# Kernel tuning notes

Hardware: AMD Instinct MI355X
Metric: run time of the kernel (lower is better)

The kernel has to match this reference:

```python
import jax, jax.numpy as jnp
import numpy as np

D_IN, N_HEADS, N_KV, HEAD_DIM = 2048, 8, 4, 256
GROUP = N_HEADS // N_KV
SCALING = 256.0 ** -0.5  # query_pre_attn_scalar = 256
EPS = 1e-6


def _rms_norm(x, gamma):
    # Gemma-style RMSNorm with (1 + gamma) scale, over last dim (head_dim)
    var = jnp.mean(x * x, axis=-1, keepdims=True)
    return x * jax.lax.rsqrt(var + EPS) * (1.0 + gamma)


def _apply_rope(x, cos, sin):
    # x: [b, h, s, d]; cos/sin: [s, d] (rotate-half convention)
    d = x.shape[-1]
    x1, x2 = x[..., : d // 2], x[..., d // 2:]
    rotated = jnp.concatenate([-x2, x1], axis=-1)
    return x * cos[None, None] + rotated * sin[None, None]


def setup_inputs() -> dict:
    key = jax.random.key(0)
    ks = jax.random.split(key, 6)
    b, s = 2, 2048
    x = jax.random.normal(ks[0], (b, s, D_IN), dtype=jnp.float32)
    # causal mask: True above diagonal = masked
    mask = jnp.triu(jnp.ones((s, s), dtype=bool), k=1)
    # RoPE tables (base 10000)
    inv_freq = 1.0 / (10000.0 ** (jnp.arange(0, HEAD_DIM, 2, dtype=jnp.float32) / HEAD_DIM))
    angles = jnp.arange(s, dtype=jnp.float32)[:, None] * inv_freq[None, :]  # [s, d/2]
    angles = jnp.concatenate([angles, angles], axis=-1)  # [s, d]
    cos, sin = jnp.cos(angles), jnp.sin(angles)
    std = 0.02
    wq = jax.random.normal(ks[1], (N_HEADS * HEAD_DIM, D_IN), dtype=jnp.float32) * std
    wk = jax.random.normal(ks[2], (N_KV * HEAD_DIM, D_IN), dtype=jnp.float32) * std
    wv = jax.random.normal(ks[3], (N_KV * HEAD_DIM, D_IN), dtype=jnp.float32) * std
    wo = jax.random.normal(ks[4], (D_IN, N_HEADS * HEAD_DIM), dtype=jnp.float32) * std
    q_gamma = jnp.zeros((HEAD_DIM,), dtype=jnp.float32)
    k_gamma = jnp.zeros((HEAD_DIM,), dtype=jnp.float32)
    return {"x": x, "mask": mask, "cos": cos, "sin": sin,
            "wq": wq, "wk": wk, "wv": wv, "wo": wo,
            "q_gamma": q_gamma, "k_gamma": k_gamma}


def reference(x, mask, cos, sin, wq, wk, wv, wo, q_gamma, k_gamma):
    b, s, _ = x.shape
    # projections (torch Linear: y = x @ W.T)
    q = (x @ wq.T).reshape(b, s, N_HEADS, HEAD_DIM).transpose(0, 2, 1, 3)  # [b,H,s,d]
    k = (x @ wk.T).reshape(b, s, N_KV, HEAD_DIM).transpose(0, 2, 1, 3)     # [b,G,s,d]
    v = (x @ wv.T).reshape(b, s, N_KV, HEAD_DIM).transpose(0, 2, 1, 3)     # [b,G,s,d]
    q = _rms_norm(q, q_gamma)
    k = _rms_norm(k, k_gamma)
    q = _apply_rope(q, cos, sin) * SCALING
    k = _apply_rope(k, cos, sin)
    # GQA via broadcast (avoids repeat_interleave): head h = g*GROUP + j (group-major)
    qg = q.reshape(b, N_KV, GROUP, s, HEAD_DIM)
    scores = jnp.einsum('bgjqd,bgkd->bgjqk', qg, k)  # [b,G,group,s,s]
    scores = jnp.where(mask[None, None, None], -jnp.inf, scores)
    weights = jax.nn.softmax(scores, axis=-1)
    ctx = jnp.einsum('bgjqk,bgkd->bgjqd', weights, v)  # [b,G,group,s,d]
    ctx = ctx.reshape(b, N_HEADS, s, HEAD_DIM).transpose(0, 2, 1, 3).reshape(b, s, N_HEADS * HEAD_DIM)
    return ctx @ wo.T
```

## Files before the change

kernel.cpp:

```cpp
#include <hip/hip_runtime.h>
#include <math.h>


typedef __bf16 bf16x8 __attribute__((ext_vector_type(8)));
typedef __bf16 bf16x4 __attribute__((ext_vector_type(4)));
typedef float  f32x4  __attribute__((ext_vector_type(4)));

#define MFMA16(a, b, c) __builtin_amdgcn_mfma_f32_16x16x32_bf16(a, b, c, 0, 0, 0)

__device__ __forceinline__ void async16(const __bf16* g, const __bf16* l) {
  __builtin_amdgcn_global_load_lds(
      (__attribute__((address_space(1))) const void*)g,
      (__attribute__((address_space(3))) void*)l, 16, 0, 0);
}

__global__ __launch_bounds__(256) void cast_f32_bf16(
    const float* __restrict__ src, __bf16* __restrict__ dst) {
  const size_t i = ((size_t)blockIdx.x * 256 + threadIdx.x) * 4;
  f32x4 v = *(const f32x4*)(src + i);
  bf16x4 o;
#pragma unroll
  for (int j = 0; j < 4; j++) o[j] = (__bf16)v[j];
  *(bf16x4*)(dst + i) = o;
}

template <typename OT>
__device__ __forceinline__ void gemm_body(const __bf16* A, const __bf16* B,
                                          OT* C, size_t m0, size_t n0,
                                          size_t ccol0, int ldc) {
  constexpr int K = 2048;
  __shared__ __align__(16) __bf16 As[128 * 32];
  __shared__ __align__(16) __bf16 Bs[128 * 32];
  const int tid = threadIdx.x;
  const int wave = tid >> 6, lane = tid & 63;
  const int lr = lane & 15, lq = lane >> 4;
  const int wm = (wave >> 1) * 64, wn = (wave & 1) * 64;

  f32x4 acc[4][4];
#pragma unroll
  for (int i = 0; i < 4; i++)
#pragma unroll
    for (int j = 0; j < 4; j++)
#pragma unroll
      for (int r = 0; r < 4; r++) acc[i][j][r] = 0.f;

  int srow[2], skof[2];
#pragma unroll
  for (int c = 0; c < 2; c++) {
    const int t = wave * 2 + c;
    const int g = t * 8 + (lane >> 3);
    const int cc = (lane & 7) ^ (g & 7);
    srow[c] = g * 2 + (cc >> 2);
    skof[c] = (cc & 3) * 8;
  }

  for (int k0 = 0; k0 < K; k0 += 32) {
#pragma unroll
    for (int c = 0; c < 2; c++) {
      const int t = wave * 2 + c;
      async16(A + (m0 + srow[c]) * K + k0 + skof[c], As + t * 512);
      async16(B + (n0 + srow[c]) * K + k0 + skof[c], Bs + t * 512);
    }
    __syncthreads();
    bf16x8 af[4], bf[4];
#pragma unroll
    for (int i = 0; i < 4; i++) {
      const int row = wm + i * 16 + lr;
      const int g = row >> 1;
      const int p = ((row & 1) * 4 + lq) ^ (g & 7);
      af[i] = *(const bf16x8*)&As[g * 64 + p * 8];
    }
#pragma unroll
    for (int j = 0; j < 4; j++) {
      const int row = wn + j * 16 + lr;
      const int g = row >> 1;
      const int p = ((row & 1) * 4 + lq) ^ (g & 7);
      bf[j] = *(const bf16x8*)&Bs[g * 64 + p * 8];
    }
#pragma unroll
    for (int i = 0; i < 4; i++)
#pragma unroll
      for (int j = 0; j < 4; j++)
        acc[i][j] = MFMA16(af[i], bf[j], acc[i][j]);
    __syncthreads();
  }

#pragma unroll
  for (int i = 0; i < 4; i++)
#pragma unroll
    for (int j = 0; j < 4; j++)
#pragma unroll
      for (int r = 0; r < 4; r++) {
        const size_t row = m0 + wm + i * 16 + lq * 4 + r;
        const size_t col = ccol0 + wn + j * 16 + lr;
        C[row * (size_t)ldc + col] = (OT)acc[i][j][r];
      }
}

template <typename OT>
__global__ __launch_bounds__(256) void gemm_bt(
    const __bf16* __restrict__ A, const __bf16* __restrict__ B,
    OT* __restrict__ C, const int ldc) {
  gemm_body<OT>(A, B, C, (size_t)blockIdx.y * 128, (size_t)blockIdx.x * 128,
                (size_t)blockIdx.x * 128, ldc);
}

__global__ __launch_bounds__(256) void gemm_qkv(
    const __bf16* __restrict__ A, const __bf16* __restrict__ Bq,
    const __bf16* __restrict__ Bk, const __bf16* __restrict__ Bv,
    __bf16* __restrict__ C) {
  const int bx = blockIdx.x;
  const __bf16* B;
  int nl;
  if (bx < 16) { B = Bq; nl = bx; }
  else if (bx < 24) { B = Bk; nl = bx - 16; }
  else { B = Bv; nl = bx - 24; }
  gemm_body<__bf16>(A, B, C, (size_t)blockIdx.y * 128, (size_t)nl * 128,
                    (size_t)bx * 128, 4096);
}

__global__ __launch_bounds__(256) void rmsrope(
    const __bf16* __restrict__ qkv, const float* __restrict__ cosb,
    const float* __restrict__ sinb, const float* __restrict__ qg,
    const float* __restrict__ kg, __bf16* __restrict__ qrot,
    __bf16* __restrict__ krot) {
  const int wave = threadIdx.x >> 6, lane = threadIdx.x & 63;
  const int rid = blockIdx.x * 4 + wave;
  const int m = rid / 12, seg = rid % 12;
  const int b = m >> 11, pos = m & 2047;
  const bool isq = seg < 8;
  const int col = isq ? seg * 256 : 2048 + (seg - 8) * 256;
  const int d = lane * 4;

  bf16x4 xv = *(const bf16x4*)(qkv + (size_t)m * 4096 + col + d);
  float x[4];
#pragma unroll
  for (int i = 0; i < 4; i++) x[i] = (float)xv[i];
  float ss = x[0] * x[0] + x[1] * x[1] + x[2] * x[2] + x[3] * x[3];
#pragma unroll
  for (int off = 1; off < 64; off <<= 1) ss += __shfl_xor(ss, off);
  const float inv = rsqrtf(ss * (1.f / 256.f) + 1e-6f);

  f32x4 gv = *(const f32x4*)((isq ? qg : kg) + d);
  float xn[4];
#pragma unroll
  for (int i = 0; i < 4; i++) xn[i] = x[i] * inv * (1.f + gv[i]);
  float rot[4];
#pragma unroll
  for (int i = 0; i < 4; i++) {
    const float pn = __shfl_xor(xn[i], 32);
    rot[i] = (lane < 32) ? -pn : pn;
  }
  f32x4 cv = *(const f32x4*)(cosb + (size_t)pos * 256 + d);
  f32x4 sv = *(const f32x4*)(sinb + (size_t)pos * 256 + d);
  const float sc = isq ? 0.0625f : 1.f;
  bf16x4 ov;
#pragma unroll
  for (int i = 0; i < 4; i++)
    ov[i] = (__bf16)((xn[i] * cv[i] + rot[i] * sv[i]) * sc);
  __bf16* dst = isq
      ? qrot + ((size_t)(b * 8 + seg) * 2048 + pos) * 256 + d
      : krot + ((size_t)(b * 4 + (seg - 8)) * 2048 + pos) * 256 + d;
  *(bf16x4*)dst = ov;
}

__global__ __launch_bounds__(256) void vtrans(const __bf16* __restrict__ qkv,
                                              __bf16* __restrict__ vT) {
  __shared__ __bf16 tile[64 * 65];
  const int bkv = blockIdx.z;
  const int d0 = blockIdx.y * 64, p0 = blockIdx.x * 64;
  const int t = threadIdx.x;
  const int b = bkv >> 2, kv = bkv & 3;
#pragma unroll
  for (int i = 0; i < 16; i++) {
    const int f = i * 256 + t;
    const int pl = f >> 6, dl = f & 63;
    tile[pl * 65 + dl] =
        qkv[(size_t)(b * 2048 + p0 + pl) * 4096 + 3072 + kv * 256 + d0 + dl];
  }
  __syncthreads();
#pragma unroll
  for (int i = 0; i < 16; i++) {
    const int f = i * 256 + t;
    const int dl = f >> 6, pl = f & 63;
    vT[((size_t)bkv * 256 + d0 + dl) * 2048 + p0 + pl] = tile[pl * 65 + dl];
  }
}

__global__ __launch_bounds__(256) void flash(
    const __bf16* __restrict__ qrot, const __bf16* __restrict__ krot,
    const __bf16* __restrict__ vT, __bf16* __restrict__ ctx) {
  __shared__ __align__(16) __bf16 Ks[2][32 * 256];
  __shared__ __align__(16) __bf16 Vs[2][256 * 32];
  __shared__ __align__(16) __bf16 Ps[4 * 1024];
  const int tid = threadIdx.x, wave = tid >> 6, lane = tid & 63;
  const int lr = lane & 15, lq = lane >> 4;
  const int bkv = blockIdx.x;
  const int b = bkv >> 2, kv = bkv & 3;
  const int qt = 31 - (int)blockIdx.y;
  const int h = kv * 2 + (wave >> 1);
  const int q0 = qt * 64 + (wave & 1) * 32;

  bf16x8 qf[2][8];
  {
    const __bf16* qbb = qrot + (size_t)(b * 8 + h) * 2048 * 256;
#pragma unroll
    for (int qi = 0; qi < 2; qi++)
#pragma unroll
      for (int i = 0; i < 8; i++)
        qf[qi][i] = *(const bf16x8*)(qbb + (size_t)(q0 + qi * 16 + lr) * 256 +
                                     i * 32 + lq * 8);
  }
  f32x4 acc[2][16];
#pragma unroll
  for (int qi = 0; qi < 2; qi++)
#pragma unroll
    for (int j = 0; j < 16; j++)
#pragma unroll
      for (int r = 0; r < 4; r++) acc[qi][j][r] = 0.f;
  float lsum[2][4];
#pragma unroll
  for (int qi = 0; qi < 2; qi++)
#pragma unroll
    for (int r = 0; r < 4; r++) lsum[qi][r] = 0.f;

  const __bf16* kbase = krot + (size_t)bkv * 2048 * 256;
  const __bf16* vbase = vT + (size_t)bkv * 256 * 2048;

  int koff[4], voff[4];
#pragma unroll
  for (int c = 0; c < 4; c++) {
    const int t = wave * 4 + c;
    {
      const int row = t * 2 + (lane >> 5);
      const int ch = (lane & 31) ^ row;
      koff[c] = row * 256 + ch * 8;
    }
    {
      const int d = t * 16 + (lane >> 2);
      const int ch = (lane & 3) ^ ((d >> 1) & 3);
      voff[c] = d * 2048 + ch * 8;
    }
  }

  const int nkt = 2 * qt + 2;
#pragma unroll
  for (int c = 0; c < 4; c++) {
    const int t = wave * 4 + c;
    async16(kbase + koff[c], &Ks[0][t * 512]);
    async16(vbase + voff[c], &Vs[0][t * 512]);
  }

  for (int kt = 0; kt < nkt; kt++) {
    const int bi = kt & 1;
    const int k0 = kt * 32;
    __syncthreads();
    if (kt + 1 < nkt) {
      const int kn = (kt + 1) * 32;
#pragma unroll
      for (int c = 0; c < 4; c++) {
        const int t = wave * 4 + c;
        async16(kbase + (size_t)kn * 256 + koff[c], &Ks[bi ^ 1][t * 512]);
        async16(vbase + kn + voff[c], &Vs[bi ^ 1][t * 512]);
      }
    }
    if (k0 <= q0 + 31) {
      f32x4 s[2][2];
#pragma unroll
      for (int qi = 0; qi < 2; qi++)
#pragma unroll
        for (int f = 0; f < 2; f++)
#pragma unroll
          for (int r = 0; r < 4; r++) s[qi][f][r] = 0.f;
#pragma unroll
      for (int i = 0; i < 8; i++) {
        bf16x8 kf0 = *(const bf16x8*)&Ks[bi][lr * 256 + (((i * 4 + lq) ^ lr) * 8)];
        bf16x8 kf1 = *(const bf16x8*)&Ks[bi][(16 + lr) * 256 +
                                            (((i * 4 + lq) ^ (16 + lr)) * 8)];
#pragma unroll
        for (int qi = 0; qi < 2; qi++) {
          s[qi][0] = MFMA16(qf[qi][i], kf0, s[qi][0]);
          s[qi][1] = MFMA16(qf[qi][i], kf1, s[qi][1]);
        }
      }
      const bool needmask = (k0 + 31 > q0);
#pragma unroll
      for (int qi = 0; qi < 2; qi++) {
        const int qa = q0 + qi * 16 + lq * 4;
#pragma unroll
        for (int f = 0; f < 2; f++) {
          const int ka = k0 + f * 16 + lr;
          const int rw = qi * 16 + lq * 4;
          const int c = f * 2 + (lr >> 3);
#pragma unroll
          for (int r = 0; r < 4; r++) {
            float p = __expf(s[qi][f][r] - 16.f);
            if (needmask && ka > qa + r) p = 0.f;
            lsum[qi][r] += p;
            const int rr = rw + r;
            Ps[wave * 1024 + rr * 32 + ((c ^ ((rr >> 1) & 3)) * 8) + (lr & 7)] =
                (__bf16)p;
          }
        }
      }
      asm volatile("s_waitcnt lgkmcnt(0)" ::: "memory");
      bf16x8 pf[2];
#pragma unroll
      for (int qi = 0; qi < 2; qi++)
        pf[qi] = *(const bf16x8*)&Ps[wave * 1024 + (qi * 16 + lr) * 32 +
                                     ((lq ^ ((lr >> 1) & 3)) * 8)];
#pragma unroll
      for (int j = 0; j < 16; j++) {
        const int d = j * 16 + lr;
        bf16x8 vf =
            *(const bf16x8*)&Vs[bi][d * 32 + ((lq ^ ((d >> 1) & 3)) * 8)];
#pragma unroll
        for (int qi = 0; qi < 2; qi++)
          acc[qi][j] = MFMA16(pf[qi], vf, acc[qi][j]);
      }
    }
  }

  float inv[2][4];
#pragma unroll
  for (int qi = 0; qi < 2; qi++)
#pragma unroll
    for (int r = 0; r < 4; r++) {
      float l = lsum[qi][r];
#pragma unroll
      for (int off = 1; off < 16; off <<= 1) l += __shfl_xor(l, off);
      inv[qi][r] = 1.f / l;
    }
#pragma unroll
  for (int qi = 0; qi < 2; qi++)
#pragma unroll
    for (int j = 0; j < 16; j++)
#pragma unroll
      for (int r = 0; r < 4; r++) {
        const int row = q0 + qi * 16 + lq * 4 + r;
        ctx[((size_t)(b * 2048 + row) * 8 + h) * 256 + j * 16 + lr] =
            (__bf16)(acc[qi][j][r] * inv[qi][r]);
      }
}

extern "C" void kernel_launch(void* const* d_in, const int* in_sizes, int n_in,
                              void* d_out, int out_size, void* d_ws,
                              size_t ws_size, hipStream_t stream) {
  const float* x = (const float*)d_in[0];
  const float* cosb = (const float*)d_in[2];
  const float* sinb = (const float*)d_in[3];
  const float* wq = (const float*)d_in[4];
  const float* wk = (const float*)d_in[5];
  const float* wv = (const float*)d_in[6];
  const float* wo = (const float*)d_in[7];
  const float* qg = (const float*)d_in[8];
  const float* kg = (const float*)d_in[9];
  float* out = (float*)d_out;

  char* ws = (char*)d_ws;
  __bf16* xbf = (__bf16*)ws;
  __bf16* wqbf = (__bf16*)(ws + ((size_t)16 << 20));
  __bf16* wkbf = (__bf16*)(ws + ((size_t)24 << 20));
  __bf16* wvbf = (__bf16*)(ws + ((size_t)28 << 20));
  __bf16* qkv = (__bf16*)(ws + ((size_t)32 << 20));
  __bf16* qrot = (__bf16*)ws;
  __bf16* krot = (__bf16*)(ws + ((size_t)16 << 20));
  __bf16* vTp = (__bf16*)(ws + ((size_t)24 << 20));
  __bf16* wobf = (__bf16*)(ws + ((size_t)32 << 20));
  __bf16* ctx = (__bf16*)(ws + ((size_t)40 << 20));

  cast_f32_bf16<<<8192, 256, 0, stream>>>(x, xbf);
  cast_f32_bf16<<<4096, 256, 0, stream>>>(wq, wqbf);
  cast_f32_bf16<<<2048, 256, 0, stream>>>(wk, wkbf);
  cast_f32_bf16<<<2048, 256, 0, stream>>>(wv, wvbf);

  gemm_qkv<<<dim3(32, 32), 256, 0, stream>>>(xbf, wqbf, wkbf, wvbf, qkv);

  rmsrope<<<12288, 256, 0, stream>>>(qkv, cosb, sinb, qg, kg, qrot, krot);
  vtrans<<<dim3(32, 4, 8), 256, 0, stream>>>(qkv, vTp);

  cast_f32_bf16<<<4096, 256, 0, stream>>>(wo, wobf);
  flash<<<dim3(8, 32), 256, 0, stream>>>(qrot, krot, vTp, ctx);

  gemm_bt<float><<<dim3(16, 32), 256, 0, stream>>>(ctx, wobf, out, 2048);
}
```

Before: 479.2 us.

## Split flash blocks per query head and drop K/V double buffering

```diff
diff --git a/kernel.cpp b/kernel.cpp
--- a/kernel.cpp
+++ b/kernel.cpp
@@ -187,19 +187,17 @@
   }
 }
 
-__global__ __launch_bounds__(256) void flash(
+__global__ __launch_bounds__(128) void flash(
     const __bf16* __restrict__ qrot, const __bf16* __restrict__ krot,
     const __bf16* __restrict__ vT, __bf16* __restrict__ ctx) {
-  __shared__ __align__(16) __bf16 Ks[2][32 * 256];
-  __shared__ __align__(16) __bf16 Vs[2][256 * 32];
-  __shared__ __align__(16) __bf16 Ps[4 * 1024];
+  __shared__ __align__(16) __bf16 Ks[32 * 256];
+  __shared__ __align__(16) __bf16 Vs[256 * 32];
+  __shared__ __align__(16) __bf16 Ps[2 * 1024];
   const int tid = threadIdx.x, wave = tid >> 6, lane = tid & 63;
   const int lr = lane & 15, lq = lane >> 4;
-  const int bkv = blockIdx.x;
-  const int b = bkv >> 2, kv = bkv & 3;
-  const int qt = 31 - (int)blockIdx.y;
-  const int h = kv * 2 + (wave >> 1);
-  const int q0 = qt * 64 + (wave & 1) * 32;
+  const int qt = 31 - (int)blockIdx.x;
+  const int h = blockIdx.y, b = blockIdx.z, kv = h >> 1;
+  const int q0 = qt * 64 + wave * 32;
 
   bf16x8 qf[2][8];
   {
@@ -224,13 +222,13 @@
 #pragma unroll
     for (int r = 0; r < 4; r++) lsum[qi][r] = 0.f;
 
-  const __bf16* kbase = krot + (size_t)bkv * 2048 * 256;
-  const __bf16* vbase = vT + (size_t)bkv * 256 * 2048;
-
-  int koff[4], voff[4];
-#pragma unroll
-  for (int c = 0; c < 4; c++) {
-    const int t = wave * 4 + c;
+  const __bf16* kbase = krot + (size_t)(b * 4 + kv) * 2048 * 256;
+  const __bf16* vbase = vT + (size_t)(b * 4 + kv) * 256 * 2048;
+
+  int koff[8], voff[8];
+#pragma unroll
+  for (int c = 0; c < 8; c++) {
+    const int t = wave * 8 + c;
     {
       const int row = t * 2 + (lane >> 5);
       const int ch = (lane & 31) ^ row;
@@ -244,26 +242,15 @@
   }
 
   const int nkt = 2 * qt + 2;
-#pragma unroll
-  for (int c = 0; c < 4; c++) {
-    const int t = wave * 4 + c;
-    async16(kbase + koff[c], &Ks[0][t * 512]);
-    async16(vbase + voff[c], &Vs[0][t * 512]);
-  }
-
   for (int kt = 0; kt < nkt; kt++) {
-    const int bi = kt & 1;
     const int k0 = kt * 32;
+#pragma unroll
+    for (int c = 0; c < 8; c++) {
+      const int t = wave * 8 + c;
+      async16(kbase + (size_t)k0 * 256 + koff[c], Ks + t * 512);
+      async16(vbase + k0 + voff[c], Vs + t * 512);
+    }
     __syncthreads();
-    if (kt + 1 < nkt) {
-      const int kn = (kt + 1) * 32;
-#pragma unroll
-      for (int c = 0; c < 4; c++) {
-        const int t = wave * 4 + c;
-        async16(kbase + (size_t)kn * 256 + koff[c], &Ks[bi ^ 1][t * 512]);
-        async16(vbase + kn + voff[c], &Vs[bi ^ 1][t * 512]);
-      }
-    }
     if (k0 <= q0 + 31) {
       f32x4 s[2][2];
 #pragma unroll
@@ -274,9 +261,9 @@
           for (int r = 0; r < 4; r++) s[qi][f][r] = 0.f;
 #pragma unroll
       for (int i = 0; i < 8; i++) {
-        bf16x8 kf0 = *(const bf16x8*)&Ks[bi][lr * 256 + (((i * 4 + lq) ^ lr) * 8)];
-        bf16x8 kf1 = *(const bf16x8*)&Ks[bi][(16 + lr) * 256 +
-                                            (((i * 4 + lq) ^ (16 + lr)) * 8)];
+        bf16x8 kf0 = *(const bf16x8*)&Ks[lr * 256 + (((i * 4 + lq) ^ lr) * 8)];
+        bf16x8 kf1 = *(const bf16x8*)&Ks[(16 + lr) * 256 +
+                                         (((i * 4 + lq) ^ (16 + lr)) * 8)];
 #pragma unroll
         for (int qi = 0; qi < 2; qi++) {
           s[qi][0] = MFMA16(qf[qi][i], kf0, s[qi][0]);
@@ -312,13 +299,13 @@
 #pragma unroll
       for (int j = 0; j < 16; j++) {
         const int d = j * 16 + lr;
-        bf16x8 vf =
-            *(const bf16x8*)&Vs[bi][d * 32 + ((lq ^ ((d >> 1) & 3)) * 8)];
+        bf16x8 vf = *(const bf16x8*)&Vs[d * 32 + ((lq ^ ((d >> 1) & 3)) * 8)];
 #pragma unroll
         for (int qi = 0; qi < 2; qi++)
           acc[qi][j] = MFMA16(pf[qi], vf, acc[qi][j]);
       }
     }
+    __syncthreads();
   }
 
   float inv[2][4];
@@ -380,7 +367,7 @@
   vtrans<<<dim3(32, 4, 8), 256, 0, stream>>>(qkv, vTp);
 
   cast_f32_bf16<<<4096, 256, 0, stream>>>(wo, wobf);
-  flash<<<dim3(8, 32), 256, 0, stream>>>(qrot, krot, vTp, ctx);
+  flash<<<dim3(32, 8, 2), 128, 0, stream>>>(qrot, krot, vTp, ctx);
 
   gemm_bt<float><<<dim3(16, 32), 256, 0, stream>>>(ctx, wobf, out, 2048);
 }
```

After: 453.7 us. -5.3%, faster.
